# Performance work log

Measured on AMD Instinct MI355X. Metric: run time of the kernel, lower is better.

The kernel has to match this reference:

```python
import jax, jax.numpy as jnp
import numpy as np
from math import ceil

N = 20000   # nodes
E = 320000  # edges
D = 128     # num_features == num_hidden
K = ceil(N * 0.1)  # 2000 PMA seeds


def _gcn(x, W, b, src, dst):
    # PyG GCNConv: add self-loops, symmetric deg^-1/2 normalization, sum-aggregate, bias
    n = x.shape[0]
    sl = jnp.arange(n)
    s = jnp.concatenate([src, sl])
    d = jnp.concatenate([dst, sl])
    deg = jax.ops.segment_sum(jnp.ones((s.shape[0],), x.dtype), d, num_segments=n)
    dinv = jax.lax.rsqrt(jnp.maximum(deg, 1e-12))
    norm = dinv[s] * dinv[d]
    h = x @ W
    return jax.ops.segment_sum(h[s] * norm[:, None], d, num_segments=n) + b


def _ln(x, g, b):
    m = jnp.mean(x, -1, keepdims=True)
    v = jnp.var(x, -1, keepdims=True)
    return (x - m) * jax.lax.rsqrt(v + 1e-5) * g + b


def setup_inputs() -> dict:
    key = jax.random.key(0)
    ks = jax.random.split(key, 32)
    w = lambda i, shape: jax.random.normal(ks[i], shape, jnp.float32) * 0.05
    z = lambda shape: jnp.zeros(shape, jnp.float32)
    o = lambda shape: jnp.ones(shape, jnp.float32)
    return {
        "x": jax.random.normal(ks[0], (N, D), jnp.float32),
        "edge_index": jax.random.randint(ks[1], (2, E), 0, N),
        "batch": jnp.zeros((N,), jnp.int32),
        "W1": w(2, (D, D)), "b1": z((D,)),
        "W2": w(3, (D, D)), "b2": z((D,)),
        "S": w(4, (1, K, D)),
        "Wq": w(5, (D, D)), "bq": z((D,)),
        "Wk": w(6, (D, D)), "bk": z((D,)),
        "Wv": w(7, (D, D)), "bv": z((D,)),
        "Wo": w(8, (D, D)), "bo": z((D,)),
        "g0": o((D,)), "be0": z((D,)),
        "g1": o((D,)), "be1": z((D,)),
        "Wl": w(9, (D, D)), "bl": z((D,)),
        "W3": w(10, (D, D)), "b3": z((D,)),
        "W4": w(11, (D, D)), "b4": z((D,)),
        "W5": w(12, (D, D)), "b5": z((D,)),
    }


def reference(x, edge_index, batch, W1, b1, W2, b2, S, Wq, bq, Wk, bk, Wv, bv,
              Wo, bo, g0, be0, g1, be1, Wl, bl, W3, b3, W4, b4, W5, b5):
    src, dst = edge_index[0], edge_index[1]
    h = jax.nn.relu(_gcn(x, W1, b1, src, dst))
    h = jax.nn.relu(_gcn(h, W2, b2, src, dst))
    # B=1 dense batch: mask all-true -> additive attention mask is 0
    Q = S @ Wq + bq                        # [1,K,D]
    Kd = _gcn(h, Wk, bk, src, dst)[None]   # [1,N,D]  (mab_conv='GCN')
    Vd = _gcn(h, Wv, bv, src, dst)[None]   # [1,N,D]
    score = jnp.einsum('bkd,bnd->bkn', Q, Kd) / jnp.sqrt(jnp.float32(D))
    A = jax.nn.softmax(score, axis=1)      # cluster=True: softmax over seed dim
    out = Q + jnp.einsum('bkn,bnd->bkd', A, Vd)
    out = _ln(out, g0, be0)
    out = out + jax.nn.relu(out @ Wo + bo)
    out = _ln(out, g1, be1)
    xl = out @ Wl + bl                     # [1,K,D]
    x_out = jnp.einsum('bkn,bkd->bnd', A, xl)[0]  # attn^T @ x -> [N,D], mask all-true
    h = jax.nn.relu(_gcn(x_out, W3, b3, src, dst))
    h = jax.nn.relu(_gcn(h, W4, b4, src, dst))
    return _gcn(h, W5, b5, src, dst)       # [N,D]
```

## Files before the change

### kernel.cpp

```cpp
#include <hip/hip_runtime.h>

#define NN 20000
#define EE 320000
#define KK 2000
#define KP 2048
#define SCALE 0.08838834764831845f
#define ZSPLIT 16
#define ACHUNKS 625
#define ZCH 4

typedef const float* cfp;
typedef __attribute__((ext_vector_type(8))) short sh8;
typedef __attribute__((ext_vector_type(4))) float f32x4;

static __device__ __forceinline__ float4 ld4(const float* p){ return *reinterpret_cast<const float4*>(p); }
static __device__ __forceinline__ void st4(float* p, float4 v){ *reinterpret_cast<float4*>(p) = v; }

static __device__ __forceinline__ unsigned short f2bf(float f){
    unsigned int u = __float_as_uint(f);
    u = (u + 0x7FFFu + ((u >> 16) & 1u)) >> 16;
    return (unsigned short)u;
}
static __device__ __forceinline__ float bf2f(unsigned short h){
    return __uint_as_float(((unsigned int)h) << 16);
}
static __device__ __forceinline__ sh8 lds8(const unsigned short* p){ return *reinterpret_cast<const sh8*>(p); }

__global__ __launch_bounds__(256) void k_count(const int* dst, int* deg){
    int i = blockIdx.x*256 + threadIdx.x;
    if (i < EE) atomicAdd(&deg[dst[i]], 1);
}

__global__ __launch_bounds__(256) void k_dinv(const int* deg, float* dinv){
    int n = blockIdx.x*256 + threadIdx.x;
    if (n < NN) dinv[n] = rsqrtf((float)deg[n] + 1.0f);
}

__global__ __launch_bounds__(1024) void k_scan(const int* cnt, int* rows){
    __shared__ int part[1024];
    int t = threadIdx.x;
    int base = t*20;
    int s = 0;
    for (int i = 0; i < 20; ++i){ int idx = base+i; if (idx < NN) s += cnt[idx]; }
    part[t] = s; __syncthreads();
    for (int off = 1; off < 1024; off <<= 1){
        int v = (t >= off) ? part[t-off] : 0;
        __syncthreads();
        part[t] += v;
        __syncthreads();
    }
    int run = part[t] - s;
    for (int i = 0; i < 20; ++i){
        int idx = base+i;
        if (idx < NN){ rows[idx] = run; run += cnt[idx]; }
    }
    if (t == 0) rows[NN] = EE;
}

__global__ __launch_bounds__(256) void k_fill(const int* src, const int* dst, const int* rows,
                                              int* cursor, int* col){
    int i = blockIdx.x*256 + threadIdx.x;
    if (i < EE){
        int d = dst[i];
        int pos = rows[d] + atomicAdd(&cursor[d], 1);
        col[pos] = src[i];
    }
}

__global__ __launch_bounds__(256) void conv_wT(cfp w0, cfp w1, cfp w2, cfp w3, cfp w4, cfp w5, cfp w6,
                                               unsigned short* wts){
    const float* in;
    switch (blockIdx.z){
        case 0: in = w0; break; case 1: in = w1; break; case 2: in = w2; break;
        case 3: in = w3; break; case 4: in = w4; break; case 5: in = w5; break;
        default: in = w6; break;
    }
    unsigned short* out = wts + (size_t)blockIdx.z*16384;
    __shared__ float t[64][65];
    int r0 = blockIdx.x*64, c0 = blockIdx.y*64;
    int tid = threadIdx.x;
    for (int i = tid; i < 64*16; i += 256){
        int r = i >> 4, c4 = (i & 15) * 4;
        float4 v = ld4(in + (size_t)(r0+r)*128 + c0 + c4);
        t[r][c4+0]=v.x; t[r][c4+1]=v.y; t[r][c4+2]=v.z; t[r][c4+3]=v.w;
    }
    __syncthreads();
    for (int i = tid; i < 64*16; i += 256){
        int c = i >> 4, r4 = (i & 15) * 4;
        ushort4 o;
        o.x = f2bf(t[r4+0][c]); o.y = f2bf(t[r4+1][c]);
        o.z = f2bf(t[r4+2][c]); o.w = f2bf(t[r4+3][c]);
        *reinterpret_cast<ushort4*>(out + (size_t)(c0+c)*128 + r0 + r4) = o;
    }
}

__global__ __launch_bounds__(512) void gemm128(const float* __restrict__ A, const float* __restrict__ Wm,
                                               float* __restrict__ C, int M,
                                               const float* bias, const float* resid, int relu){
    __shared__ __align__(16) float Ws[128*132];
    __shared__ float As[64*129];
    int tid = threadIdx.x;
    int r0 = blockIdx.x*64;
    for (int i = tid; i < 128*32; i += 512){
        int r = i >> 5, c4 = (i & 31) * 4;
        float4 v = ld4(Wm + r*128 + c4);
        st4(&Ws[r*132 + c4], v);
    }
    for (int i = tid; i < 64*32; i += 512){
        int r = i >> 5, c4 = (i & 31) * 4;
        float4 v = (r0 + r < M) ? ld4(A + (size_t)(r0+r)*128 + c4) : make_float4(0,0,0,0);
        As[r*129 + c4+0] = v.x; As[r*129 + c4+1] = v.y;
        As[r*129 + c4+2] = v.z; As[r*129 + c4+3] = v.w;
    }
    __syncthreads();
    int a = tid >> 5;
    int b = tid & 31;
    float acc[4][4] = {};
    #pragma unroll 4
    for (int d = 0; d < 128; ++d){
        float4 w = ld4(&Ws[d*132 + 4*b]);
        float wv[4] = {w.x, w.y, w.z, w.w};
        float av[4];
        #pragma unroll
        for (int i = 0; i < 4; ++i) av[i] = As[(4*a+i)*129 + d];
        #pragma unroll
        for (int i = 0; i < 4; ++i)
            #pragma unroll
            for (int j = 0; j < 4; ++j)
                acc[i][j] += av[i]*wv[j];
    }
    int cc = 4*b;
    #pragma unroll
    for (int i = 0; i < 4; ++i){
        int r = r0 + 4*a + i;
        if (r < M){
            float v[4];
            #pragma unroll
            for (int j = 0; j < 4; ++j) v[j] = acc[i][j];
            if (bias){
                #pragma unroll
                for (int j = 0; j < 4; ++j) v[j] += bias[cc+j];
            }
            if (relu){
                #pragma unroll
                for (int j = 0; j < 4; ++j) v[j] = fmaxf(v[j], 0.f);
            }
            if (resid){
                float4 rv = ld4(resid + (size_t)r*128 + cc);
                v[0]+=rv.x; v[1]+=rv.y; v[2]+=rv.z; v[3]+=rv.w;
            }
            st4(C + (size_t)r*128 + cc, make_float4(v[0],v[1],v[2],v[3]));
        }
    }
}

__global__ __launch_bounds__(256) void tgemm(const unsigned short* __restrict__ A, int M,
                                             const unsigned short* __restrict__ Wt,
                                             const float* __restrict__ rscale,
                                             unsigned short* __restrict__ C){
    int tid = threadIdx.x;
    int wave = tid >> 6, lane = tid & 63;
    int wm = wave >> 1, wn = wave & 1;
    int m_base = blockIdx.x*64 + wm*32;
    int n_base = blockIdx.y*64 + wn*32;
    int l15 = lane & 15;
    int roff = (lane >> 4) * 8;
    const unsigned short* ap0 = A + (size_t)(m_base + l15)*128 + roff;
    const unsigned short* ap1 = ap0 + 16*128;
    const unsigned short* b0p = Wt + (size_t)(n_base + l15)*128 + roff;
    const unsigned short* b1p = b0p + 16*128;
    f32x4 acc00 = (f32x4)0.f, acc01 = (f32x4)0.f, acc10 = (f32x4)0.f, acc11 = (f32x4)0.f;
    #pragma unroll
    for (int r = 0; r < 128; r += 32){
        sh8 a0 = lds8(ap0 + r);
        sh8 a1 = lds8(ap1 + r);
        sh8 b0 = lds8(b0p + r);
        sh8 b1 = lds8(b1p + r);
        acc00 = __builtin_amdgcn_mfma_f32_16x16x32_bf16(a0, b0, acc00, 0, 0, 0);
        acc01 = __builtin_amdgcn_mfma_f32_16x16x32_bf16(a0, b1, acc01, 0, 0, 0);
        acc10 = __builtin_amdgcn_mfma_f32_16x16x32_bf16(a1, b0, acc10, 0, 0, 0);
        acc11 = __builtin_amdgcn_mfma_f32_16x16x32_bf16(a1, b1, acc11, 0, 0, 0);
    }
    int rq = (lane >> 4) * 4;
    f32x4 accs[2][2] = {{acc00, acc01},{acc10, acc11}};
    #pragma unroll
    for (int mi = 0; mi < 2; ++mi){
        #pragma unroll
        for (int ni = 0; ni < 2; ++ni){
            f32x4 a = accs[mi][ni];
            int gn = n_base + ni*16 + l15;
            #pragma unroll
            for (int reg = 0; reg < 4; ++reg){
                int gm = m_base + mi*16 + rq + reg;
                if (gm < M) C[(size_t)gm*128 + gn] = f2bf(a[reg] * (rscale ? rscale[gm] : 1.f));
            }
        }
    }
}

__global__ __launch_bounds__(256) void gcn_agg_bf(const unsigned short* __restrict__ y, const float* __restrict__ dinv,
                                                  const int* __restrict__ rows, const int* __restrict__ col,
                                                  const float* __restrict__ bias, void* __restrict__ outv,
                                                  int relu, int out_fp32){
    int wid = (int)((blockIdx.x*256 + threadIdx.x) >> 6);
    int lane = threadIdx.x & 63;
    if (wid >= NN) return;
    int f = lane*2;
    ushort2 u = *reinterpret_cast<const ushort2*>(y + (size_t)wid*128 + f);
    float ax = bf2f(u.x), ay = bf2f(u.y);
    int s = rows[wid], e = rows[wid+1];
    int j = s;
    int e8 = s + ((e - s) & ~7);
    for (; j < e8; j += 8){
        ushort2 v[8];
        #pragma unroll
        for (int q = 0; q < 8; ++q){
            int c = col[j+q];
            v[q] = *reinterpret_cast<const ushort2*>(y + (size_t)c*128 + f);
        }
        #pragma unroll
        for (int q = 0; q < 8; ++q){ ax += bf2f(v[q].x); ay += bf2f(v[q].y); }
    }
    for (; j < e; ++j){
        int c0 = col[j];
        ushort2 v0 = *reinterpret_cast<const ushort2*>(y + (size_t)c0*128 + f);
        ax += bf2f(v0.x); ay += bf2f(v0.y);
    }
    float dn = dinv[wid];
    float ox = ax*dn + bias[f];
    float oy = ay*dn + bias[f+1];
    if (relu){ ox = fmaxf(ox, 0.f); oy = fmaxf(oy, 0.f); }
    if (out_fp32){
        *reinterpret_cast<float2*>((float*)outv + (size_t)wid*128 + f) = make_float2(ox, oy);
    } else {
        ushort2 o; o.x = f2bf(ox); o.y = f2bf(oy);
        *reinterpret_cast<ushort2*>((unsigned short*)outv + (size_t)wid*128 + f) = o;
    }
}

__global__ __launch_bounds__(256) void conv_bf16(const float* __restrict__ in, unsigned short* __restrict__ out, int n4){
    int i = blockIdx.x*256 + threadIdx.x;
    if (i < n4){
        float4 v = ld4(in + (size_t)i*4);
        ushort4 o;
        o.x = f2bf(v.x); o.y = f2bf(v.y); o.z = f2bf(v.z); o.w = f2bf(v.w);
        *reinterpret_cast<ushort4*>(out + (size_t)i*4) = o;
    }
}

__global__ __launch_bounds__(256) void conv_bf16_T(const float* __restrict__ in, unsigned short* __restrict__ out,
                                                   int M, int ldout, const float* __restrict__ rscale){
    __shared__ float t[64][65];
    int r0 = blockIdx.x*64, c0 = blockIdx.y*64;
    int tid = threadIdx.x;
    for (int i = tid; i < 64*16; i += 256){
        int r = i >> 4, c4 = (i & 15) * 4;
        float4 v = (r0 + r < M) ? ld4(in + (size_t)(r0+r)*128 + c0 + c4) : make_float4(0,0,0,0);
        if (rscale && r0 + r < M){
            float sc = rscale[r0 + r];
            v.x *= sc; v.y *= sc; v.z *= sc; v.w *= sc;
        }
        t[r][c4+0]=v.x; t[r][c4+1]=v.y; t[r][c4+2]=v.z; t[r][c4+3]=v.w;
    }
    __syncthreads();
    for (int i = tid; i < 64*16; i += 256){
        int c = i >> 4, r4 = (i & 15) * 4;
        if (r0 + r4 < M){
            ushort4 o;
            o.x = f2bf(t[r4+0][c]); o.y = f2bf(t[r4+1][c]);
            o.z = f2bf(t[r4+2][c]); o.w = f2bf(t[r4+3][c]);
            *reinterpret_cast<ushort4*>(out + (size_t)(c0+c)*ldout + r0 + r4) = o;
        }
    }
}

__global__ __launch_bounds__(256) void k_rcp32(const float* __restrict__ zp, const float* __restrict__ dinv,
                                               float* __restrict__ zinv, float* __restrict__ zdinv){
    int n = blockIdx.x*256 + threadIdx.x;
    if (n < NN){
        float s = 0.f;
        #pragma unroll
        for (int y = 0; y < ZCH; ++y) s += zp[(size_t)y*NN + n];
        float zi = 1.f / s;
        zinv[n] = zi;
        zdinv[n] = zi * dinv[n];
    }
}

__global__ __launch_bounds__(256) void s_gemm_exp(const unsigned short* __restrict__ Kb,
                                                  const unsigned short* __restrict__ Qb2,
                                                  unsigned short* __restrict__ E, float* __restrict__ zpart){
    __shared__ unsigned short Es[64*68];
    __shared__ float zsh[2][64];
    int tid = threadIdx.x;
    int wave = tid >> 6, lane = tid & 63;
    int wm = wave >> 1, wn = wave & 1;
    int n_blk = blockIdx.x*64;
    int k_base = blockIdx.y*512;
    int l15 = lane & 15;
    int roff = (lane >> 4) * 8;
    int rq = (lane >> 4) * 4;
    const unsigned short* ap0 = Kb + (size_t)(n_blk + wm*32 + l15)*128 + roff;
    const unsigned short* ap1 = ap0 + 16*128;
    sh8 a0[4], a1[4];
    #pragma unroll
    for (int r = 0; r < 4; ++r){ a0[r] = lds8(ap0 + r*32); a1[r] = lds8(ap1 + r*32); }
    const unsigned short* qbase = Qb2 + (size_t)(k_base + wn*32 + l15)*128 + roff;
    sh8 q0[4], q1[4];
    #pragma unroll
    for (int r = 0; r < 4; ++r){ q0[r] = lds8(qbase + r*32); q1[r] = lds8(qbase + 16*128 + r*32); }
    float zacc[2][4] = {{0.f,0.f,0.f,0.f},{0.f,0.f,0.f,0.f}};
    for (int kb = 0; kb < 8; ++kb){
        sh8 n0[4], n1[4];
        if (kb < 7){
            const unsigned short* qn = qbase + (size_t)(kb+1)*64*128;
            #pragma unroll
            for (int r = 0; r < 4; ++r){ n0[r] = lds8(qn + r*32); n1[r] = lds8(qn + 16*128 + r*32); }
        } else {
            #pragma unroll
            for (int r = 0; r < 4; ++r){ n0[r] = (sh8)0; n1[r] = (sh8)0; }
        }
        f32x4 acc00 = (f32x4)0.f, acc01 = (f32x4)0.f, acc10 = (f32x4)0.f, acc11 = (f32x4)0.f;
        #pragma unroll
        for (int r = 0; r < 4; ++r){
            acc00 = __builtin_amdgcn_mfma_f32_16x16x32_bf16(a0[r], q0[r], acc00, 0, 0, 0);
            acc01 = __builtin_amdgcn_mfma_f32_16x16x32_bf16(a0[r], q1[r], acc01, 0, 0, 0);
            acc10 = __builtin_amdgcn_mfma_f32_16x16x32_bf16(a1[r], q0[r], acc10, 0, 0, 0);
            acc11 = __builtin_amdgcn_mfma_f32_16x16x32_bf16(a1[r], q1[r], acc11, 0, 0, 0);
        }
        __syncthreads();
        int kcol = k_base + kb*64;
        f32x4 accs[2][2] = {{acc00, acc01},{acc10, acc11}};
        #pragma unroll
        for (int mi = 0; mi < 2; ++mi){
            #pragma unroll
            for (int ni = 0; ni < 2; ++ni){
                f32x4 a = accs[mi][ni];
                int c_loc = wn*32 + ni*16 + l15;
                bool kv = (kcol + c_loc) < KK;
                #pragma unroll
                for (int reg = 0; reg < 4; ++reg){
                    float e = kv ? __expf(a[reg]*SCALE) : 0.f;
                    Es[(wm*32 + mi*16 + rq + reg)*68 + c_loc] = f2bf(e);
                    zacc[mi][reg] += e;
                }
            }
        }
        __syncthreads();
        for (int i = tid; i < 512; i += 256){
            int r = i >> 3, c8 = (i & 7) * 8;
            if (n_blk + r < NN){
                ushort4 lo = *reinterpret_cast<const ushort4*>(&Es[r*68 + c8]);
                ushort4 hi = *reinterpret_cast<const ushort4*>(&Es[r*68 + c8 + 4]);
                unsigned short* dst = E + (size_t)(n_blk + r)*KP + kcol + c8;
                *reinterpret_cast<ushort4*>(dst) = lo;
                *reinterpret_cast<ushort4*>(dst + 4) = hi;
            }
        }
        #pragma unroll
        for (int r = 0; r < 4; ++r){ q0[r] = n0[r]; q1[r] = n1[r]; }
    }
    #pragma unroll
    for (int mi = 0; mi < 2; ++mi){
        #pragma unroll
        for (int reg = 0; reg < 4; ++reg){
            float v = zacc[mi][reg];
            v += __shfl_xor(v, 1);
            v += __shfl_xor(v, 2);
            v += __shfl_xor(v, 4);
            v += __shfl_xor(v, 8);
            zacc[mi][reg] = v;
        }
    }
    if (l15 == 0){
        int h = lane >> 4;
        #pragma unroll
        for (int mi = 0; mi < 2; ++mi)
            #pragma unroll
            for (int reg = 0; reg < 4; ++reg)
                zsh[wn][wm*32 + mi*16 + h*4 + reg] = zacc[mi][reg];
    }
    __syncthreads();
    if (tid < 64){
        int n = n_blk + tid;
        if (n < NN) zpart[(size_t)blockIdx.y*NN + n] = zsh[0][tid] + zsh[1][tid];
    }
}

__global__ __launch_bounds__(256) void attn_gemm(const unsigned short* __restrict__ E,
                                                 const unsigned short* __restrict__ Vt,
                                                 float* __restrict__ part){
    __shared__ unsigned short As[64*36];
    int tid = threadIdx.x;
    int wave = tid >> 6, lane = tid & 63;
    int kk0 = blockIdx.x*64;
    int per = (ACHUNKS + ZSPLIT - 1) / ZSPLIT;
    int c0 = blockIdx.y*per;
    int c1 = min(ACHUNKS, c0 + per);
    int l15 = lane & 15;
    int q8 = (lane >> 4) * 8;
    int d0 = wave*32;
    int n_l = tid & 31;
    int k8 = (tid >> 5) * 8;
    f32x4 acc[4][2];
    #pragma unroll
    for (int g = 0; g < 4; ++g){ acc[g][0] = (f32x4)0.f; acc[g][1] = (f32x4)0.f; }
    const unsigned short* ebase = E + (size_t)n_l*KP + kk0 + k8;
    const unsigned short* vb0p = Vt + (size_t)(d0 + l15)*NN + q8;
    const unsigned short* vb1p = vb0p + (size_t)16*NN;
    sh8 etmp = lds8(ebase + (size_t)c0*32*KP);
    sh8 vb0 = lds8(vb0p + c0*32);
    sh8 vb1 = lds8(vb1p + c0*32);
    for (int ch = c0; ch < c1; ++ch){
        unsigned short tmp[8];
        *reinterpret_cast<sh8*>(tmp) = etmp;
        #pragma unroll
        for (int j = 0; j < 8; ++j) As[(k8 + j)*36 + n_l] = tmp[j];
        __syncthreads();
        sh8 etn = (sh8)0, vbn0 = (sh8)0, vbn1 = (sh8)0;
        if (ch + 1 < c1){
            etn  = lds8(ebase + (size_t)(ch+1)*32*KP);
            vbn0 = lds8(vb0p + (ch+1)*32);
            vbn1 = lds8(vb1p + (ch+1)*32);
        }
        #pragma unroll
        for (int g = 0; g < 4; ++g){
            const unsigned short* ap = &As[(g*16 + l15)*36 + q8];
            union { struct { ushort4 lo, hi; } u; sh8 v; } af;
            af.u.lo = *reinterpret_cast<const ushort4*>(ap);
            af.u.hi = *reinterpret_cast<const ushort4*>(ap + 4);
            acc[g][0] = __builtin_amdgcn_mfma_f32_16x16x32_bf16(af.v, vb0, acc[g][0], 0, 0, 0);
            acc[g][1] = __builtin_amdgcn_mfma_f32_16x16x32_bf16(af.v, vb1, acc[g][1], 0, 0, 0);
        }
        __syncthreads();
        etmp = etn; vb0 = vbn0; vb1 = vbn1;
    }
    float* pbase = part + (size_t)blockIdx.y*KK*128;
    int rq = (lane >> 4) * 4;
    #pragma unroll
    for (int g = 0; g < 4; ++g){
        #pragma unroll
        for (int ni = 0; ni < 2; ++ni){
            int d = d0 + ni*16 + l15;
            #pragma unroll
            for (int reg = 0; reg < 4; ++reg){
                int kk = kk0 + g*16 + rq + reg;
                if (kk < KK) pbase[(size_t)kk*128 + d] = acc[g][ni][reg];
            }
        }
    }
}

__global__ __launch_bounds__(256) void xout_gemm(const unsigned short* __restrict__ E,
                                                 const unsigned short* __restrict__ B,
                                                 float* __restrict__ xpart){
    int tid = threadIdx.x;
    int wave = tid >> 6, lane = tid & 63;
    int m_base = blockIdx.x*32;
    int kz = blockIdx.y*1024;
    int l15 = lane & 15;
    int roff = (lane >> 4) * 8;
    int rq = (lane >> 4) * 4;
    const unsigned short* ap0 = E + (size_t)(m_base + l15)*KP + kz + roff;
    const unsigned short* ap1 = ap0 + (size_t)16*KP;
    const unsigned short* bp0 = B + (size_t)(wave*32 + l15)*KP + kz + roff;
    const unsigned short* bp1 = bp0 + (size_t)16*KP;
    f32x4 acc[2][2];
    #pragma unroll
    for (int mi = 0; mi < 2; ++mi)
        #pragma unroll
        for (int ni = 0; ni < 2; ++ni) acc[mi][ni] = (f32x4)0.f;
    sh8 a_[2][2], b_[2][2];
    a_[0][0]=lds8(ap0);    a_[0][1]=lds8(ap0+32);
    a_[1][0]=lds8(ap1);    a_[1][1]=lds8(ap1+32);
    b_[0][0]=lds8(bp0);    b_[0][1]=lds8(bp0+32);
    b_[1][0]=lds8(bp1);    b_[1][1]=lds8(bp1+32);
    for (int r = 0; r < 1024; r += 64){
        int rn = r + 64;
        sh8 na[2][2], nb[2][2];
        if (rn < 1024){
            na[0][0]=lds8(ap0+rn);    na[0][1]=lds8(ap0+rn+32);
            na[1][0]=lds8(ap1+rn);    na[1][1]=lds8(ap1+rn+32);
            nb[0][0]=lds8(bp0+rn);    nb[0][1]=lds8(bp0+rn+32);
            nb[1][0]=lds8(bp1+rn);    nb[1][1]=lds8(bp1+rn+32);
        } else {
            #pragma unroll
            for (int mi = 0; mi < 2; ++mi){ na[mi][0] = (sh8)0; na[mi][1] = (sh8)0; }
            #pragma unroll
            for (int ni = 0; ni < 2; ++ni){ nb[ni][0] = (sh8)0; nb[ni][1] = (sh8)0; }
        }
        #pragma unroll
        for (int h = 0; h < 2; ++h){
            #pragma unroll
            for (int mi = 0; mi < 2; ++mi)
                #pragma unroll
                for (int ni = 0; ni < 2; ++ni)
                    acc[mi][ni] = __builtin_amdgcn_mfma_f32_16x16x32_bf16(a_[mi][h], b_[ni][h], acc[mi][ni], 0, 0, 0);
        }
        #pragma unroll
        for (int mi = 0; mi < 2; ++mi){ a_[mi][0] = na[mi][0]; a_[mi][1] = na[mi][1]; }
        #pragma unroll
        for (int ni = 0; ni < 2; ++ni){ b_[ni][0] = nb[ni][0]; b_[ni][1] = nb[ni][1]; }
    }
    float* pbase = xpart + (size_t)blockIdx.y*NN*128;
    #pragma unroll
    for (int mi = 0; mi < 2; ++mi){
        #pragma unroll
        for (int ni = 0; ni < 2; ++ni){
            f32x4 a = acc[mi][ni];
            int d = wave*32 + ni*16 + l15;
            #pragma unroll
            for (int reg = 0; reg < 4; ++reg){
                int gm = m_base + mi*16 + rq + reg;
                if (gm < NN) pbase[(size_t)gm*128 + d] = a[reg];
            }
        }
    }
}

__global__ __launch_bounds__(256) void xred(const float* __restrict__ xp, const float* __restrict__ zdinv,
                                            unsigned short* __restrict__ out){
    int i = blockIdx.x*256 + threadIdx.x;
    if (i < NN*32){
        int row = i >> 5;
        float4 p0 = ld4(xp + (size_t)i*4);
        float4 p1 = ld4(xp + (size_t)NN*128 + (size_t)i*4);
        float sc = zdinv[row];
        ushort4 o;
        o.x = f2bf((p0.x + p1.x)*sc);
        o.y = f2bf((p0.y + p1.y)*sc);
        o.z = f2bf((p0.z + p1.z)*sc);
        o.w = f2bf((p0.w + p1.w)*sc);
        *reinterpret_cast<ushort4*>(out + (size_t)i*4) = o;
    }
}

__global__ __launch_bounds__(128) void ln_ker(const float* __restrict__ in, int nparts,
                                              const float* __restrict__ resid,
                                              const float* __restrict__ g, const float* __restrict__ be,
                                              float* __restrict__ out){
    __shared__ float rs[128], rq[128];
    int r = blockIdx.x, t = threadIdx.x;
    float v = 0.f;
    for (int p = 0; p < nparts; ++p) v += in[(size_t)p*KK*128 + r*128 + t];
    if (resid) v += resid[r*128 + t];
    rs[t] = v; rq[t] = v*v;
    __syncthreads();
    for (int off = 64; off > 0; off >>= 1){
        if (t < off){ rs[t] += rs[t+off]; rq[t] += rq[t+off]; }
        __syncthreads();
    }
    float mean = rs[0]*(1.f/128.f);
    float var = rq[0]*(1.f/128.f) - mean*mean;
    out[r*128 + t] = (v - mean)*rsqrtf(var + 1e-5f)*g[t] + be[t];
}

extern "C" void kernel_launch(void* const* d_in, const int* in_sizes, int n_in,
                              void* d_out, int out_size, void* d_ws, size_t ws_size,
                              hipStream_t stream){
    cfp x  = (cfp)d_in[0];
    const int* ei = (const int*)d_in[1];
    const int* esrc = ei;
    const int* edst = ei + EE;
    cfp W1=(cfp)d_in[3], b1=(cfp)d_in[4], W2=(cfp)d_in[5], b2=(cfp)d_in[6];
    cfp S =(cfp)d_in[7];
    cfp Wq=(cfp)d_in[8],  bq=(cfp)d_in[9],  Wk=(cfp)d_in[10], bk=(cfp)d_in[11];
    cfp Wv=(cfp)d_in[12], bv=(cfp)d_in[13], Wo=(cfp)d_in[14], bo=(cfp)d_in[15];
    cfp g0=(cfp)d_in[16], be0=(cfp)d_in[17], g1=(cfp)d_in[18], be1=(cfp)d_in[19];
    cfp Wl=(cfp)d_in[20], bl=(cfp)d_in[21], W3=(cfp)d_in[22], b3=(cfp)d_in[23];
    cfp W4=(cfp)d_in[24], b4=(cfp)d_in[25], W5=(cfp)d_in[26], b5=(cfp)d_in[27];

    char* wsb = (char*)d_ws;
    const size_t MB = 1048576;
    int*   deg    = (int*)  (wsb + 0);
    float* dinv   = (float*)(wsb + 81920);
    int*   rows   = (int*)  (wsb + 163840);
    int*   cursor = (int*)  (wsb + 245760);
    int*   col    = (int*)  (wsb + 327680);
    float* Qb     = (float*)(wsb + 2*MB);
    float* o1     = (float*)(wsb + 3*MB);
    float* o2     = (float*)(wsb + 4*MB);
    float* o3     = (float*)(wsb + 5*MB);
    float* xlb    = (float*)(wsb + 6*MB);
    float* zpart  = (float*)(wsb + 7*MB);
    float* zinv   = (float*)(wsb + 10*MB);
    float* zdinv  = (float*)(wsb + 10*MB + 131072);
    unsigned short* Wts  = (unsigned short*)(wsb + 10*MB + 262144);
    unsigned short* Qbf  = (unsigned short*)(wsb + 11*MB);
    unsigned short* xlt3 = (unsigned short*)(wsb + 11*MB + 524288);
    unsigned short* xbf = (unsigned short*)(wsb + 12*MB);
    unsigned short* h1  = (unsigned short*)(wsb + 17*MB);
    unsigned short* h2  = (unsigned short*)(wsb + 22*MB);
    unsigned short* ybuf= (unsigned short*)(wsb + 27*MB);
    unsigned short* Kbf = (unsigned short*)(wsb + 32*MB);
    unsigned short* Vtz = (unsigned short*)(wsb + 37*MB);
    float* NB3    = (float*)(wsb + 42*MB);
    float* part   = (float*)(wsb + 42*MB);
    float* xpart  = (float*)(wsb + 42*MB);
    unsigned short* E = (unsigned short*)(wsb + 62*MB);
    float* outp   = (float*)d_out;
    unsigned short* h3 = xbf;
    unsigned short* h4 = h1;

    (void)hipMemsetAsync(deg, 0, NN*sizeof(int), stream);
    (void)hipMemsetAsync(cursor, 0, NN*sizeof(int), stream);
    (void)hipMemsetAsync(xlt3, 0, 128*KP*sizeof(unsigned short), stream);

    k_count<<<1250, 256, 0, stream>>>(edst, deg);
    k_dinv<<<79, 256, 0, stream>>>(deg, dinv);
    k_scan<<<1, 1024, 0, stream>>>(deg, rows);
    k_fill<<<1250, 256, 0, stream>>>(esrc, edst, rows, cursor, col);

    conv_wT<<<dim3(2,2,7), 256, 0, stream>>>(W1, W2, Wk, Wv, W3, W4, W5, Wts);
    conv_bf16<<<2500, 256, 0, stream>>>(x, xbf, NN*32);
    unsigned short* W1t = Wts;
    unsigned short* W2t = Wts + 16384;
    unsigned short* Wkt = Wts + 2*16384;
    unsigned short* Wvt = Wts + 3*16384;
    unsigned short* W4t = Wts + 5*16384;
    unsigned short* W5t = Wts + 6*16384;

    const int GN = 313;
    const int GK = 32;

    tgemm<<<dim3(GN,2), 256, 0, stream>>>(xbf, NN, W1t, dinv, ybuf);
    gcn_agg_bf<<<5000, 256, 0, stream>>>(ybuf, dinv, rows, col, b1, h1, 1, 0);
    tgemm<<<dim3(GN,2), 256, 0, stream>>>(h1, NN, W2t, dinv, ybuf);
    gcn_agg_bf<<<5000, 256, 0, stream>>>(ybuf, dinv, rows, col, b2, h2, 1, 0);
    tgemm<<<dim3(GN,2), 256, 0, stream>>>(h2, NN, Wkt, dinv, ybuf);
    gcn_agg_bf<<<5000, 256, 0, stream>>>(ybuf, dinv, rows, col, bk, Kbf, 0, 0);
    gemm128<<<GK, 512, 0, stream>>>(S, Wq, Qb, KK, bq, nullptr, 0);
    conv_bf16<<<250, 256, 0, stream>>>(Qb, Qbf, KK*32);
    s_gemm_exp<<<dim3(GN, ZCH), 256, 0, stream>>>(Kbf, Qbf, E, zpart);
    k_rcp32<<<79, 256, 0, stream>>>(zpart, dinv, zinv, zdinv);
    tgemm<<<dim3(GN,2), 256, 0, stream>>>(h2, NN, Wvt, dinv, ybuf);
    gcn_agg_bf<<<5000, 256, 0, stream>>>(ybuf, dinv, rows, col, bv, NB3, 0, 1);
    conv_bf16_T<<<dim3(GN, 2), 256, 0, stream>>>(NB3, Vtz, NN, NN, zinv);
    attn_gemm<<<dim3(GK, ZSPLIT), 256, 0, stream>>>(E, Vtz, part);
    ln_ker<<<KK, 128, 0, stream>>>(part, ZSPLIT, Qb, g0, be0, o1);
    gemm128<<<GK, 512, 0, stream>>>(o1, Wo, o2, KK, bo, o1, 1);
    ln_ker<<<KK, 128, 0, stream>>>(o2, 1, nullptr, g1, be1, o3);
    gemm128<<<GK, 512, 0, stream>>>(o3, Wl, xlb, KK, bl, nullptr, 0);
    gemm128<<<GK, 512, 0, stream>>>(xlb, W3, o1, KK, nullptr, nullptr, 0);
    conv_bf16_T<<<dim3(GK, 2), 256, 0, stream>>>(o1, xlt3, KK, KP, nullptr);
    xout_gemm<<<dim3(625, 2), 256, 0, stream>>>(E, xlt3, xpart);
    xred<<<2500, 256, 0, stream>>>(xpart, zdinv, ybuf);
    gcn_agg_bf<<<5000, 256, 0, stream>>>(ybuf, dinv, rows, col, b3, h3, 1, 0);
    tgemm<<<dim3(GN,2), 256, 0, stream>>>(h3, NN, W4t, dinv, ybuf);
    gcn_agg_bf<<<5000, 256, 0, stream>>>(ybuf, dinv, rows, col, b4, h4, 1, 0);
    tgemm<<<dim3(GN,2), 256, 0, stream>>>(h4, NN, W5t, dinv, ybuf);
    gcn_agg_bf<<<5000, 256, 0, stream>>>(ybuf, dinv, rows, col, b5, outp, 0, 1);
}
```

Baseline: 609.1 us.

## Fuse x_out split-K reduction into GEMM with LDS-staged swizzled E tiles

The xout GEMM no longer splits the K dimension into two partial fp32 buffers followed by a separate reduction kernel. It now runs the full K range in one block and applies the zdinv scale and bf16 conversion in the epilogue, so the xred kernel and its fp32 partial traffic go away. E tiles are staged into double-buffered, XOR-swizzled LDS with global_load_lds, and B fragments are prefetched in registers. The trade-off is half as many blocks (625), which means less parallelism, plus per-tile barriers.

```diff
diff --git a/kernel.cpp b/kernel.cpp
--- a/kernel.cpp
+++ b/kernel.cpp
@@ -25,6 +25,12 @@
     return __uint_as_float(((unsigned int)h) << 16);
 }
 static __device__ __forceinline__ sh8 lds8(const unsigned short* p){ return *reinterpret_cast<const sh8*>(p); }
+
+static __device__ __forceinline__ void stage16(const unsigned short* g, unsigned short* l){
+    __builtin_amdgcn_global_load_lds(
+        (const __attribute__((address_space(1))) unsigned int*)g,
+        (__attribute__((address_space(3))) unsigned int*)l, 16, 0, 0);
+}
 
 __global__ __launch_bounds__(256) void k_count(const int* dst, int* deg){
     int i = blockIdx.x*256 + threadIdx.x;
@@ -453,56 +459,75 @@
 
 __global__ __launch_bounds__(256) void xout_gemm(const unsigned short* __restrict__ E,
                                                  const unsigned short* __restrict__ B,
-                                                 float* __restrict__ xpart){
+                                                 const float* __restrict__ zdinv,
+                                                 unsigned short* __restrict__ out){
+    __shared__ __align__(16) unsigned short ebuf[2][4096];
     int tid = threadIdx.x;
     int wave = tid >> 6, lane = tid & 63;
+    int l15 = lane & 15;
+    int h = lane >> 4;
     int m_base = blockIdx.x*32;
-    int kz = blockIdx.y*1024;
-    int l15 = lane & 15;
-    int roff = (lane >> 4) * 8;
-    int rq = (lane >> 4) * 4;
-    const unsigned short* ap0 = E + (size_t)(m_base + l15)*KP + kz + roff;
-    const unsigned short* ap1 = ap0 + (size_t)16*KP;
-    const unsigned short* bp0 = B + (size_t)(wave*32 + l15)*KP + kz + roff;
+    int srow0 = wave*4 + h;
+    int skb0  = (l15*16) ^ ((srow0 & 15) << 4);
+    int srow1 = 16 + srow0;
+    int skb1  = (l15*16) ^ ((srow1 & 15) << 4);
+    const unsigned short* g0 = E + (size_t)(m_base + srow0)*KP + (skb0 >> 1);
+    const unsigned short* g1 = E + (size_t)(m_base + srow1)*KP + (skb1 >> 1);
+    unsigned short* l0 = &ebuf[0][wave*512];
+    unsigned short* l1 = &ebuf[1][wave*512];
+    const unsigned short* bp0 = B + (size_t)(wave*32 + l15)*KP + h*8;
     const unsigned short* bp1 = bp0 + (size_t)16*KP;
+    int rswz = l15 << 4;
+
     f32x4 acc[2][2];
     #pragma unroll
     for (int mi = 0; mi < 2; ++mi)
         #pragma unroll
         for (int ni = 0; ni < 2; ++ni) acc[mi][ni] = (f32x4)0.f;
-    sh8 a_[2][2], b_[2][2];
-    a_[0][0]=lds8(ap0);    a_[0][1]=lds8(ap0+32);
-    a_[1][0]=lds8(ap1);    a_[1][1]=lds8(ap1+32);
-    b_[0][0]=lds8(bp0);    b_[0][1]=lds8(bp0+32);
-    b_[1][0]=lds8(bp1);    b_[1][1]=lds8(bp1+32);
-    for (int r = 0; r < 1024; r += 64){
-        int rn = r + 64;
-        sh8 na[2][2], nb[2][2];
-        if (rn < 1024){
-            na[0][0]=lds8(ap0+rn);    na[0][1]=lds8(ap0+rn+32);
-            na[1][0]=lds8(ap1+rn);    na[1][1]=lds8(ap1+rn+32);
-            nb[0][0]=lds8(bp0+rn);    nb[0][1]=lds8(bp0+rn+32);
-            nb[1][0]=lds8(bp1+rn);    nb[1][1]=lds8(bp1+rn+32);
+
+    stage16(g0, l0);
+    stage16(g1, l0 + 2048);
+    sh8 b0[4], b1[4];
+    #pragma unroll
+    for (int s = 0; s < 4; ++s){ b0[s] = lds8(bp0 + s*32); b1[s] = lds8(bp1 + s*32); }
+    __syncthreads();
+
+    for (int t = 0; t < 16; ++t){
+        if (t < 15){
+            const unsigned short* ng0 = g0 + (t+1)*128;
+            const unsigned short* ng1 = g1 + (t+1)*128;
+            unsigned short* nl = (t & 1) ? l0 : l1;
+            stage16(ng0, nl);
+            stage16(ng1, nl + 2048);
+        }
+        sh8 nb0[4], nb1[4];
+        if (t < 15){
+            #pragma unroll
+            for (int s = 0; s < 4; ++s){
+                nb0[s] = lds8(bp0 + (t+1)*128 + s*32);
+                nb1[s] = lds8(bp1 + (t+1)*128 + s*32);
+            }
         } else {
             #pragma unroll
-            for (int mi = 0; mi < 2; ++mi){ na[mi][0] = (sh8)0; na[mi][1] = (sh8)0; }
-            #pragma unroll
-            for (int ni = 0; ni < 2; ++ni){ nb[ni][0] = (sh8)0; nb[ni][1] = (sh8)0; }
-        }
-        #pragma unroll
-        for (int h = 0; h < 2; ++h){
-            #pragma unroll
-            for (int mi = 0; mi < 2; ++mi)
-                #pragma unroll
-                for (int ni = 0; ni < 2; ++ni)
-                    acc[mi][ni] = __builtin_amdgcn_mfma_f32_16x16x32_bf16(a_[mi][h], b_[ni][h], acc[mi][ni], 0, 0, 0);
-        }
-        #pragma unroll
-        for (int mi = 0; mi < 2; ++mi){ a_[mi][0] = na[mi][0]; a_[mi][1] = na[mi][1]; }
-        #pragma unroll
-        for (int ni = 0; ni < 2; ++ni){ b_[ni][0] = nb[ni][0]; b_[ni][1] = nb[ni][1]; }
-    }
-    float* pbase = xpart + (size_t)blockIdx.y*NN*128;
+            for (int s = 0; s < 4; ++s){ nb0[s] = (sh8)0; nb1[s] = (sh8)0; }
+        }
+        const unsigned short* eb = (t & 1) ? ebuf[1] : ebuf[0];
+        #pragma unroll
+        for (int s = 0; s < 4; ++s){
+            int ko = ((h*16 + s*64) ^ rswz) >> 1;
+            sh8 a0 = lds8(eb + l15*128 + ko);
+            sh8 a1 = lds8(eb + (16 + l15)*128 + ko);
+            acc[0][0] = __builtin_amdgcn_mfma_f32_16x16x32_bf16(a0, b0[s], acc[0][0], 0, 0, 0);
+            acc[0][1] = __builtin_amdgcn_mfma_f32_16x16x32_bf16(a0, b1[s], acc[0][1], 0, 0, 0);
+            acc[1][0] = __builtin_amdgcn_mfma_f32_16x16x32_bf16(a1, b0[s], acc[1][0], 0, 0, 0);
+            acc[1][1] = __builtin_amdgcn_mfma_f32_16x16x32_bf16(a1, b1[s], acc[1][1], 0, 0, 0);
+        }
+        __syncthreads();
+        #pragma unroll
+        for (int s = 0; s < 4; ++s){ b0[s] = nb0[s]; b1[s] = nb1[s]; }
+    }
+
+    int rq = h*4;
     #pragma unroll
     for (int mi = 0; mi < 2; ++mi){
         #pragma unroll
@@ -512,26 +537,9 @@
             #pragma unroll
             for (int reg = 0; reg < 4; ++reg){
                 int gm = m_base + mi*16 + rq + reg;
-                if (gm < NN) pbase[(size_t)gm*128 + d] = a[reg];
-            }
-        }
-    }
-}
-
-__global__ __launch_bounds__(256) void xred(const float* __restrict__ xp, const float* __restrict__ zdinv,
-                                            unsigned short* __restrict__ out){
-    int i = blockIdx.x*256 + threadIdx.x;
-    if (i < NN*32){
-        int row = i >> 5;
-        float4 p0 = ld4(xp + (size_t)i*4);
-        float4 p1 = ld4(xp + (size_t)NN*128 + (size_t)i*4);
-        float sc = zdinv[row];
-        ushort4 o;
-        o.x = f2bf((p0.x + p1.x)*sc);
-        o.y = f2bf((p0.y + p1.y)*sc);
-        o.z = f2bf((p0.z + p1.z)*sc);
-        o.w = f2bf((p0.w + p1.w)*sc);
-        *reinterpret_cast<ushort4*>(out + (size_t)i*4) = o;
+                out[(size_t)gm*128 + d] = f2bf(a[reg] * zdinv[gm]);
+            }
+        }
     }
 }
 
@@ -596,7 +604,6 @@
     unsigned short* Vtz = (unsigned short*)(wsb + 37*MB);
     float* NB3    = (float*)(wsb + 42*MB);
     float* part   = (float*)(wsb + 42*MB);
-    float* xpart  = (float*)(wsb + 42*MB);
     unsigned short* E = (unsigned short*)(wsb + 62*MB);
     float* outp   = (float*)d_out;
     unsigned short* h3 = xbf;
@@ -643,8 +650,7 @@
     gemm128<<<GK, 512, 0, stream>>>(o3, Wl, xlb, KK, bl, nullptr, 0);
     gemm128<<<GK, 512, 0, stream>>>(xlb, W3, o1, KK, nullptr, nullptr, 0);
     conv_bf16_T<<<dim3(GK, 2), 256, 0, stream>>>(o1, xlt3, KK, KP, nullptr);
-    xout_gemm<<<dim3(625, 2), 256, 0, stream>>>(E, xlt3, xpart);
-    xred<<<2500, 256, 0, stream>>>(xpart, zdinv, ybuf);
+    xout_gemm<<<625, 256, 0, stream>>>(E, xlt3, zdinv, ybuf);
     gcn_agg_bf<<<5000, 256, 0, stream>>>(ybuf, dinv, rows, col, b3, h3, 1, 0);
     tgemm<<<dim3(GN,2), 256, 0, stream>>>(h3, NN, W4t, dinv, ybuf);
     gcn_agg_bf<<<5000, 256, 0, stream>>>(ybuf, dinv, rows, col, b4, h4, 1, 0);
```

Measured after the change: 581.0 us. 1.05x faster.
